# Kernel optimization log

Measured on AMD Instinct MI355X. Metric: run time of the kernel, lower is better.

Reference implementation:

```python
import jax, jax.numpy as jnp
import numpy as np

T, N = 32, 256
HID, NL = 64, 1
D_CH, Hg, Wg = 2, 8, 8            # obs shape (2, 8, 8); d must be 2 to match Conv2d(2*HID, 2*HID)
NSUB, SUBDIM = 6, 3               # subtasks shape (n_subtasks, subtask_dim)
OBS_V, SUB_V, NACT = 16, 20, 6    # vocab sizes; action_space.n = NSUB
OBS_LEN = D_CH * Hg * Wg          # 128
SUB_LEN = NSUB * SUBDIM           # 18
GRU_IN = HID * (OBS_LEN + SUBDIM) # 8384
STATE = 2 + NL * HID + NACT + NSUB  # a(1)+v(1)+h(64)+a_probs(6)+p(6) = 78


def setup_inputs() -> dict:
    key = jax.random.key(0)
    ks = jax.random.split(key, 12)
    obs_idx = jax.random.randint(ks[0], (T, N, OBS_LEN), 0, OBS_V)
    sub_idx = jax.random.randint(ks[1], (T, N, SUB_LEN), 0, SUB_V)
    act = jax.random.randint(ks[2], (T, N, 1), 0, NACT)  # all >= 0 -> sample_new is a no-op
    inputs = jnp.concatenate([obs_idx, sub_idx, act], -1).astype(jnp.float32)
    hx = jnp.zeros((1, N, STATE), jnp.float32)  # all-zero -> new_episode everywhere
    sd = lambda f: 1.0 / np.sqrt(f)
    return dict(
        inputs=inputs,
        hx=hx,
        subtask_emb=jax.random.normal(ks[3], (SUB_V, HID)),
        obs_emb=jax.random.normal(ks[4], (OBS_V, HID)),
        conv_w=jax.random.normal(ks[5], (2 * HID, 2 * HID)) * sd(2 * HID),
        conv_b=jnp.zeros((2 * HID,)),
        w_ih=jax.random.normal(ks[6], (3 * HID, GRU_IN)) * sd(GRU_IN),
        w_hh=jax.random.normal(ks[7], (3 * HID, HID)) * sd(HID),
        b_ih=jnp.zeros((3 * HID,)),
        b_hh=jnp.zeros((3 * HID,)),
        critic_w=jax.random.normal(ks[8], (1, HID)) * sd(HID),
        critic_b=jnp.zeros((1,)),
        phi_w=jax.random.normal(ks[9], (1, HID)) * sd(HID),
        phi_b=jnp.zeros((1,)),
    )


def _forward(inputs, hx, subtask_emb, obs_emb, conv_w, conv_b, w_ih, w_hh,
             b_ih, b_hh, critic_w, critic_b, phi_w, phi_b):
    ints = inputs.astype(jnp.int32)
    obs_all = ints[:, :, :OBS_LEN]                      # (T,N,128)
    sub_all = ints[:, :, OBS_LEN:OBS_LEN + SUB_LEN]     # (T,N,18)
    act_all = ints[:, :, -1]                            # (T,N)

    # subtask memory from first timestep: (N, NSUB, SUBDIM*HID)
    M = subtask_emb[sub_all[0]].reshape(N, NSUB, SUBDIM * HID)

    hx0 = hx[0]
    new_episode = jnp.all(hx0 == 0, axis=-1)            # (N,)
    # recurrent state split order a(1), v(1), h(NL*HID), a_probs(NACT), p(NSUB)
    h0 = hx0[:, 2:2 + NL * HID].reshape(N, NL, HID).transpose(1, 0, 2)  # (NL,N,HID)
    p0 = hx0[:, 2 + NL * HID + NACT:]
    p0 = p0.at[:, 0].set(jnp.where(new_episode, 1.0, p0[:, 0]))

    def gru_cell(x, h):
        gx = x @ w_ih.T + b_ih
        gh = h @ w_hh.T + b_hh
        r = jax.nn.sigmoid(gx[:, :HID] + gh[:, :HID])
        z = jax.nn.sigmoid(gx[:, HID:2 * HID] + gh[:, HID:2 * HID])
        n = jnp.tanh(gx[:, 2 * HID:] + r * gh[:, 2 * HID:])
        return (1 - z) * n + z * h

    def step(carry, xt):
        h, p = carry
        obs_t, act_t = xt
        r_vec = jnp.einsum('ns,nsk->nk', p, M)          # (p.unsqueeze(1) @ M).squeeze(1)
        emb = obs_emb[obs_t.reshape(N, D_CH, Hg, Wg)]   # (N,2,H,W,HID)
        conv_in = emb.transpose(0, 1, 4, 2, 3).reshape(N, 2 * HID, Hg * Wg)
        conv_out = jnp.einsum('ncp,oc->nop', conv_in, conv_w) + conv_b[None, :, None]  # 1x1 conv
        gru_in = jnp.concatenate([conv_out.reshape(N, -1), r_vec], -1)
        hn = gru_cell(gru_in, h[0])                     # single-layer GRU, seq len 1
        h_new = hn[None]
        c = jax.nn.sigmoid(hn @ phi_w.T + phi_b)        # (N,1)
        # torch.roll(F.pad(p,(0,1)), 1) flattened: pad column is 0, so this is a
        # right-shift with 0 fill; p1[:, -1] == p[:, -1].
        p1 = jnp.concatenate([jnp.zeros((N, 1), p.dtype), p[:, :-1]], axis=1)
        p2 = p1 + p * p[:, -1:]
        p_new = (1 - c) * p + c * p2
        probs = p_new / p_new.sum(-1, keepdims=True)    # FixedCategorical(p).probs
        v = hn @ critic_w.T + critic_b                  # (N,1)
        a = act_t.astype(jnp.float32)[:, None]          # actions all >=0 -> no resampling
        h_flat = h_new.transpose(1, 0, 2).reshape(N, -1)
        ys = jnp.concatenate([a, v, h_flat, probs, p_new], -1)
        return (h_new, p_new), ys

    _, hx_out = jax.lax.scan(step, (h0, p0), (obs_all, act_all))  # (T,N,78)
    return hx_out


def reference(inputs, hx, subtask_emb, obs_emb, conv_w, conv_b, w_ih, w_hh,
              b_ih, b_hh, critic_w, critic_b, phi_w, phi_b):
    hx_out = _forward(inputs, hx, subtask_emb, obs_emb, conv_w, conv_b, w_ih,
                      w_hh, b_ih, b_hh, critic_w, critic_b, phi_w, phi_b)
    return (hx_out, hx_out[-1:])
```

## Files before the change

kernel.cpp:

```cpp
#include <hip/hip_runtime.h>
#include <hip/hip_bf16.h>
#include <math.h>

#define TT 32
#define NN 256
#define HID 64
#define OBS_LEN 128
#define SUB_LEN 18
#define IN_ROW 147
#define GJ 192
#define GRU_IN 8384
#define STATE 78
#define NSUB 6
#define NT_TILES 1572

typedef __fp16 half2_t __attribute__((ext_vector_type(2)));

__device__ __forceinline__ float sigm(float x) {
    return 1.0f / (1.0f + __expf(-x));
}

__device__ __forceinline__ unsigned short f2bf(float f) {
    unsigned u = __float_as_uint(f);
    u += 0x7fffu + ((u >> 16) & 1u);
    return (unsigned short)(u >> 16);
}

#if defined(__has_builtin)
#if __has_builtin(__builtin_amdgcn_fdot2)
#define HAVE_FDOT2 1
#endif
#endif

__device__ __forceinline__ float fdot2(half2_t a, half2_t b, float c) {
#ifdef HAVE_FDOT2
    return __builtin_amdgcn_fdot2(a, b, c, false);
#else
    return fmaf((float)a.x, (float)b.x, fmaf((float)a.y, (float)b.y, c));
#endif
}

__global__ __launch_bounds__(256) void k_TGC(const float* __restrict__ w_ih,
                                             const float* __restrict__ obs_emb,
                                             const float* __restrict__ conv_w,
                                             const float* __restrict__ conv_b,
                                             const float* __restrict__ b_ih,
                                             float* __restrict__ wT,
                                             float* __restrict__ G,
                                             float* __restrict__ CB2) {
    int b = blockIdx.x;
    int tid = threadIdx.x;
    __shared__ float tile[32][33];
    __shared__ float red[4];

    if (b < NT_TILES) {
        int bx = b % 262, by = b / 262;
        int i0 = bx * 32, j0 = by * 32;
        int tx = tid & 31, ty = tid >> 5;
        #pragma unroll
        for (int a = 0; a < 4; a++)
            tile[ty + a * 8][tx] = w_ih[(size_t)(j0 + ty + a * 8) * GRU_IN + i0 + tx];
        __syncthreads();
        #pragma unroll
        for (int a = 0; a < 4; a++)
            wT[(size_t)(i0 + ty + a * 8) * GJ + j0 + tx] = tile[tx][ty + a * 8];
    } else if (b < NT_TILES + 16) {
        int i = (b - NT_TILES) * 256 + tid;
        int v = i & 15, d = (i >> 4) & 1, o = i >> 5;
        float acc = 0.f;
        const float* oe = obs_emb + v * 64;
        const float* cw = conv_w + o * 128 + d * 64;
        #pragma unroll
        for (int hd = 0; hd < 64; hd++) acc = fmaf(oe[hd], cw[hd], acc);
        G[i] = acc;
    } else {
        int j = b - (NT_TILES + 16);
        const float* wr = w_ih + (size_t)j * GRU_IN;
        float acc = 0.f;
        #pragma unroll 8
        for (int i = tid; i < 8192; i += 256) acc = fmaf(conv_b[i >> 6], wr[i], acc);
        for (int off = 32; off > 0; off >>= 1) acc += __shfl_down(acc, off, 64);
        if ((tid & 63) == 0) red[tid >> 6] = acc;
        __syncthreads();
        if (tid == 0) CB2[j] = b_ih[j] + red[0] + red[1] + red[2] + red[3];
    }
}

__global__ __launch_bounds__(192) void k_EQ(const float* __restrict__ inputs,
                                            const float* __restrict__ subtask_emb,
                                            const float* __restrict__ G,
                                            const float* __restrict__ wT,
                                            unsigned short* __restrict__ E16,
                                            float* __restrict__ Q) {
    int b = blockIdx.x;
    int j = threadIdx.x;

    if (b < 256) {
        int dp = b >> 1, half = b & 1;
        int d = dp >> 6, p = dp & 63;
        __shared__ __align__(16) float Gs[128 * 8];
        for (int e = j; e < 1024; e += GJ) {
            int o = e >> 3, vv = e & 7;
            Gs[e] = G[(o << 5) + (d << 4) + (half << 3) + vv];
        }
        __syncthreads();
        float acc[8];
        #pragma unroll
        for (int v = 0; v < 8; v++) acc[v] = 0.f;
        const float* wb = wT + (size_t)p * GJ + j;
        #pragma unroll 8
        for (int o = 0; o < 128; o++) {
            float w = wb[(size_t)(o * 64) * GJ];
            float4 g0 = *(const float4*)&Gs[o * 8];
            float4 g1 = *(const float4*)&Gs[o * 8 + 4];
            acc[0] = fmaf(g0.x, w, acc[0]);
            acc[1] = fmaf(g0.y, w, acc[1]);
            acc[2] = fmaf(g0.z, w, acc[2]);
            acc[3] = fmaf(g0.w, w, acc[3]);
            acc[4] = fmaf(g1.x, w, acc[4]);
            acc[5] = fmaf(g1.y, w, acc[5]);
            acc[6] = fmaf(g1.z, w, acc[6]);
            acc[7] = fmaf(g1.w, w, acc[7]);
        }
        unsigned short* Eo = E16 + ((size_t)(dp * 16 + half * 8)) * GJ;
        #pragma unroll
        for (int v = 0; v < 8; v++) Eo[v * GJ + j] = f2bf(acc[v]);
    } else {
        int n = b - 256;
        __shared__ int sidx[SUB_LEN];
        __shared__ __align__(16) float Ms[GJ * 8];
        if (j < SUB_LEN) sidx[j] = (int)inputs[(size_t)n * IN_ROW + OBS_LEN + j];
        __syncthreads();
        for (int e = j; e < NSUB * GJ; e += GJ) {
            int s = e / GJ, k = e - s * GJ;
            int row = sidx[s * 3 + (k >> 6)];
            Ms[k * 8 + s] = subtask_emb[row * 64 + (k & 63)];
        }
        __syncthreads();
        float acc[NSUB] = {0.f, 0.f, 0.f, 0.f, 0.f, 0.f};
        const float* base = wT + (size_t)8192 * GJ + j;
        #pragma unroll 8
        for (int k = 0; k < GJ; k++) {
            float w = base[(size_t)k * GJ];
            float4 m0 = *(const float4*)&Ms[k * 8];
            float2 m1 = *(const float2*)&Ms[k * 8 + 4];
            acc[0] = fmaf(m0.x, w, acc[0]);
            acc[1] = fmaf(m0.y, w, acc[1]);
            acc[2] = fmaf(m0.z, w, acc[2]);
            acc[3] = fmaf(m0.w, w, acc[3]);
            acc[4] = fmaf(m1.x, w, acc[4]);
            acc[5] = fmaf(m1.y, w, acc[5]);
        }
        for (int s = 0; s < NSUB; s++) Q[((size_t)n * NSUB + s) * GJ + j] = acc[s];
    }
}

__global__ __launch_bounds__(192) void k_gx(const float* __restrict__ inputs,
                                            const unsigned short* __restrict__ E16,
                                            const float* __restrict__ CB2,
                                            float* __restrict__ gx_all) {
    int tn0 = blockIdx.x * 4;
    int tid = threadIdx.x;
    __shared__ int idx[4][OBS_LEN];
    for (int e = tid; e < 4 * OBS_LEN; e += 192)
        idx[e >> 7][e & 127] = (int)inputs[(size_t)(tn0 + (e >> 7)) * IN_ROW + (e & 127)];
    __syncthreads();
    int r = tid / 48, l = tid - r * 48;
    int jj = l * 4;
    int tn = tn0 + r;
    float4 cb = *(const float4*)(CB2 + jj);
    float a0 = cb.x, a1 = cb.y, a2 = cb.z, a3 = cb.w;
    const int* id = idx[r];
    #pragma unroll 16
    for (int dp = 0; dp < OBS_LEN; dp++) {
        uint2 u = *(const uint2*)(E16 + ((size_t)(dp * 16 + id[dp])) * GJ + jj);
        a0 += __uint_as_float(u.x << 16);
        a1 += __uint_as_float(u.x & 0xffff0000u);
        a2 += __uint_as_float(u.y << 16);
        a3 += __uint_as_float(u.y & 0xffff0000u);
    }
    float4 o4; o4.x = a0; o4.y = a1; o4.z = a2; o4.w = a3;
    *(float4*)(gx_all + (size_t)tn * GJ + jj) = o4;
}

__global__ __launch_bounds__(64, 1) void k_rec(const float* __restrict__ inputs,
                                               const float* __restrict__ hx,
                                               const float* __restrict__ w_hh,
                                               const float* __restrict__ b_hh,
                                               const float* __restrict__ critic_w,
                                               const float* __restrict__ critic_b,
                                               const float* __restrict__ phi_w,
                                               const float* __restrict__ phi_b,
                                               const float* __restrict__ Q,
                                               const float* __restrict__ gx_all,
                                               float* __restrict__ out) {
    int n = blockIdx.x;
    int lane = threadIdx.x;

    __shared__ __align__(16) float gx_lds[TT * GJ];
    __shared__ __align__(16) __fp16 h16[64];
    __shared__ float act_sh[TT];

    for (int e = lane * 4; e < TT * GJ; e += 64 * 4) {
        int t = e / GJ, j = e - t * GJ;
        *(float4*)&gx_lds[e] = *(const float4*)(gx_all + ((size_t)t * NN + n) * GJ + j);
    }
    if (lane < TT)
        act_sh[lane] = inputs[((size_t)lane * NN + n) * IN_ROW + (IN_ROW - 1)];

    half2_t wv0[32], wv1[32], wv2[32];
    {
        const float4* r0 = (const float4*)(w_hh + (size_t)lane * 64);
        const float4* r1 = (const float4*)(w_hh + (size_t)(64 + lane) * 64);
        const float4* r2 = (const float4*)(w_hh + (size_t)(128 + lane) * 64);
        #pragma unroll
        for (int h4 = 0; h4 < 16; h4++) {
            float4 a = r0[h4];
            wv0[2*h4]   = __builtin_amdgcn_cvt_pkrtz(a.x, a.y);
            wv0[2*h4+1] = __builtin_amdgcn_cvt_pkrtz(a.z, a.w);
            float4 c = r1[h4];
            wv1[2*h4]   = __builtin_amdgcn_cvt_pkrtz(c.x, c.y);
            wv1[2*h4+1] = __builtin_amdgcn_cvt_pkrtz(c.z, c.w);
            float4 d = r2[h4];
            wv2[2*h4]   = __builtin_amdgcn_cvt_pkrtz(d.x, d.y);
            wv2[2*h4+1] = __builtin_amdgcn_cvt_pkrtz(d.z, d.w);
        }
    }
    half2_t ph[32];
    {
        const float4* pp = (const float4*)phi_w;
        #pragma unroll
        for (int h4 = 0; h4 < 16; h4++) {
            float4 a = pp[h4];
            ph[2*h4]   = __builtin_amdgcn_cvt_pkrtz(a.x, a.y);
            ph[2*h4+1] = __builtin_amdgcn_cvt_pkrtz(a.z, a.w);
        }
    }
    float q0[NSUB], q1[NSUB], q2[NSUB];
    #pragma unroll
    for (int s = 0; s < NSUB; s++) {
        const float* qb = Q + ((size_t)n * NSUB + s) * GJ;
        q0[s] = qb[lane]; q1[s] = qb[64 + lane]; q2[s] = qb[128 + lane];
    }
    float bh0 = b_hh[lane], bh1 = b_hh[64 + lane], bh2 = b_hh[128 + lane];
    float cw_own = critic_w[lane];
    float phib = phi_b[0], crtb = critic_b[0];

    float v0 = hx[(size_t)n * STATE + lane];
    float v1 = (lane < STATE - 64) ? hx[(size_t)n * STATE + 64 + lane] : 0.f;
    unsigned long long bal0 = __ballot(v0 != 0.f);
    unsigned long long bal1 = __ballot((lane < STATE - 64) && v1 != 0.f);
    bool ne = ((bal0 | bal1) == 0ULL);
    float h_own = hx[(size_t)n * STATE + 2 + lane];
    float p0, p1, p2, p3, p4, p5;
    {
        const float* pb = hx + (size_t)n * STATE + 72;
        p0 = pb[0]; p1 = pb[1]; p2 = pb[2]; p3 = pb[3]; p4 = pb[4]; p5 = pb[5];
    }
    if (ne) p0 = 1.0f;
    h16[lane] = (__fp16)h_own;

    float vlast = 0.f;

    auto finalize = [&](int tf, float pc) {
        float c = sigm(pc + phib);
        float n0 = fmaf(c, (p0 * p5)      - p0, p0);
        float n1 = fmaf(c, (p0 + p1 * p5) - p1, p1);
        float n2 = fmaf(c, (p1 + p2 * p5) - p2, p2);
        float n3 = fmaf(c, (p2 + p3 * p5) - p3, p3);
        float n4 = fmaf(c, (p3 + p4 * p5) - p4, p4);
        float n5 = fmaf(c, (p4 + p5 * p5) - p5, p5);
        float psum = ((n0 + n1) + (n2 + n3)) + (n4 + n5);
        float rinv = 1.0f / psum;
        if (lane < 12) {
            int s = (lane < 6) ? lane : lane - 6;
            float pp = n0;
            pp = (s == 1) ? n1 : pp;
            pp = (s == 2) ? n2 : pp;
            pp = (s == 3) ? n3 : pp;
            pp = (s == 4) ? n4 : pp;
            pp = (s == 5) ? n5 : pp;
            size_t fb = ((size_t)tf * NN + n) * STATE;
            out[fb + ((lane < 6) ? (72 + lane) : (66 + lane - 6))] =
                (lane < 6) ? pp : pp * rinv;
        }
        p0 = n0; p1 = n1; p2 = n2; p3 = n3; p4 = n4; p5 = n5;
    };

    for (int t = 0; t < TT; t++) {
        uint4 raw[8];
        #pragma unroll
        for (int rix = 0; rix < 8; rix++) raw[rix] = ((const uint4*)h16)[rix];
        half2_t h2[32];
        {
            const unsigned* rw = (const unsigned*)raw;
            #pragma unroll
            for (int k = 0; k < 32; k++) h2[k] = __builtin_bit_cast(half2_t, rw[k]);
        }

        float A0 = 0.f, B0 = 0.f, A1 = 0.f, B1 = 0.f, A2 = 0.f, B2 = 0.f;
        float PA = 0.f, PB = 0.f;
        #pragma unroll
        for (int k = 0; k < 16; k++) {
            A0 = fdot2(h2[k], wv0[k], A0);
            B0 = fdot2(h2[16 + k], wv0[16 + k], B0);
            A1 = fdot2(h2[k], wv1[k], A1);
            B1 = fdot2(h2[16 + k], wv1[16 + k], B1);
            A2 = fdot2(h2[k], wv2[k], A2);
            B2 = fdot2(h2[16 + k], wv2[16 + k], B2);
            PA = fdot2(h2[k], ph[k], PA);
            PB = fdot2(h2[16 + k], ph[16 + k], PB);
        }
        float pc = PA + PB;

        if (t > 0) finalize(t - 1, pc);

        float gx0 = gx_lds[t * GJ + lane];
        float gx1 = gx_lds[t * GJ + 64 + lane];
        float gx2 = gx_lds[t * GJ + 128 + lane];
        gx0 = fmaf(p0, q0[0], gx0); gx1 = fmaf(p0, q1[0], gx1); gx2 = fmaf(p0, q2[0], gx2);
        gx0 = fmaf(p1, q0[1], gx0); gx1 = fmaf(p1, q1[1], gx1); gx2 = fmaf(p1, q2[1], gx2);
        gx0 = fmaf(p2, q0[2], gx0); gx1 = fmaf(p2, q1[2], gx1); gx2 = fmaf(p2, q2[2], gx2);
        gx0 = fmaf(p3, q0[3], gx0); gx1 = fmaf(p3, q1[3], gx1); gx2 = fmaf(p3, q2[3], gx2);
        gx0 = fmaf(p4, q0[4], gx0); gx1 = fmaf(p4, q1[4], gx1); gx2 = fmaf(p4, q2[4], gx2);
        gx0 = fmaf(p5, q0[5], gx0); gx1 = fmaf(p5, q1[5], gx1); gx2 = fmaf(p5, q2[5], gx2);

        float gh0 = bh0 + A0 + B0;
        float gh1 = bh1 + A1 + B1;
        float gh2 = bh2 + A2 + B2;

        float r = sigm(gx0 + gh0);
        float z = sigm(gx1 + gh1);
        float x2 = fmaf(r, gh2, gx2);
        float e2 = __expf(2.f * x2);
        float nv = 1.f - 2.f / (e2 + 1.f);
        float hn = fmaf(z, h_own - nv, nv);

        size_t base = ((size_t)t * NN + n) * STATE;
        out[base + 2 + lane] = hn;
        float vc = hn * cw_own;
        #pragma unroll
        for (int off = 32; off > 0; off >>= 1) vc += __shfl_xor(vc, off, 64);
        vlast = vc + crtb;
        if (lane == 0) out[base + 1] = vlast;
        else if (lane == 1) out[base + 0] = act_sh[t];

        h16[lane] = (__fp16)hn;
        h_own = hn;
    }

    {
        uint4 raw[8];
        #pragma unroll
        for (int rix = 0; rix < 8; rix++) raw[rix] = ((const uint4*)h16)[rix];
        const unsigned* rw = (const unsigned*)raw;
        float PA = 0.f, PB = 0.f;
        #pragma unroll
        for (int k = 0; k < 16; k++) {
            PA = fdot2(__builtin_bit_cast(half2_t, rw[k]), ph[k], PA);
            PB = fdot2(__builtin_bit_cast(half2_t, rw[16 + k]), ph[16 + k], PB);
        }
        finalize(TT - 1, PA + PB);
        float psum = ((p0 + p1) + (p2 + p3)) + (p4 + p5);
        float rinv = 1.0f / psum;
        size_t fs = (size_t)TT * NN * STATE + (size_t)n * STATE;
        out[fs + 2 + lane] = h_own;
        if (lane < 12) {
            int s = (lane < 6) ? lane : lane - 6;
            float pp = p0;
            pp = (s == 1) ? p1 : pp;
            pp = (s == 2) ? p2 : pp;
            pp = (s == 3) ? p3 : pp;
            pp = (s == 4) ? p4 : pp;
            pp = (s == 5) ? p5 : pp;
            out[fs + ((lane < 6) ? (72 + lane) : (66 + lane - 6))] =
                (lane < 6) ? pp : pp * rinv;
        } else if (lane == 12) {
            out[fs + 0] = act_sh[TT - 1];
        } else if (lane == 13) {
            out[fs + 1] = vlast;
        }
    }
}

extern "C" void kernel_launch(void* const* d_in, const int* in_sizes, int n_in,
                              void* d_out, int out_size, void* d_ws, size_t ws_size,
                              hipStream_t stream) {
    const float* inputs      = (const float*)d_in[0];
    const float* hx          = (const float*)d_in[1];
    const float* subtask_emb = (const float*)d_in[2];
    const float* obs_emb     = (const float*)d_in[3];
    const float* conv_w      = (const float*)d_in[4];
    const float* conv_b      = (const float*)d_in[5];
    const float* w_ih        = (const float*)d_in[6];
    const float* w_hh        = (const float*)d_in[7];
    const float* b_ih        = (const float*)d_in[8];
    const float* b_hh        = (const float*)d_in[9];
    const float* critic_w    = (const float*)d_in[10];
    const float* critic_b    = (const float*)d_in[11];
    const float* phi_w       = (const float*)d_in[12];
    const float* phi_b       = (const float*)d_in[13];
    float* out = (float*)d_out;

    float* ws   = (float*)d_ws;
    float* wT   = ws;
    float* G    = wT + (size_t)GRU_IN * GJ;
    float* CB2  = G + 4096;
    float* Ef   = CB2 + 192;
    unsigned short* E16 = (unsigned short*)Ef;
    float* Q    = Ef + 196608;
    float* gx   = Q + (size_t)NN * NSUB * GJ;

    k_TGC<<<NT_TILES + 16 + GJ, 256, 0, stream>>>(w_ih, obs_emb, conv_w, conv_b,
                                                  b_ih, wT, G, CB2);
    k_EQ<<<512, GJ, 0, stream>>>(inputs, subtask_emb, G, wT, E16, Q);
    k_gx<<<TT * NN / 4, GJ, 0, stream>>>(inputs, E16, CB2, gx);
    k_rec<<<NN, 64, 0, stream>>>(inputs, hx, w_hh, b_hh, critic_w, critic_b,
                                 phi_w, phi_b, Q, gx, out);
}
```

Measured before the change: 178.3 us.

## Precompute gather byte offsets in k_gx and defer critic reduction out of recurrence

```diff
diff --git a/kernel.cpp b/kernel.cpp
--- a/kernel.cpp
+++ b/kernel.cpp
@@ -161,25 +161,66 @@
                                             float* __restrict__ gx_all) {
     int tn0 = blockIdx.x * 4;
     int tid = threadIdx.x;
-    __shared__ int idx[4][OBS_LEN];
-    for (int e = tid; e < 4 * OBS_LEN; e += 192)
-        idx[e >> 7][e & 127] = (int)inputs[(size_t)(tn0 + (e >> 7)) * IN_ROW + (e & 127)];
+    __shared__ __align__(16) int off[4][OBS_LEN];
+    for (int e = tid; e < 4 * OBS_LEN; e += 192) {
+        int row = e >> 7, dp = e & 127;
+        int id = (int)inputs[(size_t)(tn0 + row) * IN_ROW + dp];
+        off[row][dp] = (dp * 16 + id) * 384;
+    }
     __syncthreads();
     int r = tid / 48, l = tid - r * 48;
     int jj = l * 4;
     int tn = tn0 + r;
-    float4 cb = *(const float4*)(CB2 + jj);
-    float a0 = cb.x, a1 = cb.y, a2 = cb.z, a3 = cb.w;
-    const int* id = idx[r];
-    #pragma unroll 16
-    for (int dp = 0; dp < OBS_LEN; dp++) {
-        uint2 u = *(const uint2*)(E16 + ((size_t)(dp * 16 + id[dp])) * GJ + jj);
-        a0 += __uint_as_float(u.x << 16);
-        a1 += __uint_as_float(u.x & 0xffff0000u);
-        a2 += __uint_as_float(u.y << 16);
-        a3 += __uint_as_float(u.y & 0xffff0000u);
-    }
-    float4 o4; o4.x = a0; o4.y = a1; o4.z = a2; o4.w = a3;
+    const char* base = (const char*)E16 + jj * 2;
+    float2 acc0 = *(const float2*)(CB2 + jj);
+    float2 acc1 = *(const float2*)(CB2 + jj + 2);
+    const int* id = off[r];
+    #pragma unroll
+    for (int dq = 0; dq < 16; dq++) {
+        int4 o0 = *(const int4*)&id[dq * 8];
+        int4 o1 = *(const int4*)&id[dq * 8 + 4];
+        uint2 u0 = *(const uint2*)(base + o0.x);
+        uint2 u1 = *(const uint2*)(base + o0.y);
+        uint2 u2 = *(const uint2*)(base + o0.z);
+        uint2 u3 = *(const uint2*)(base + o0.w);
+        uint2 u4 = *(const uint2*)(base + o1.x);
+        uint2 u5 = *(const uint2*)(base + o1.y);
+        uint2 u6 = *(const uint2*)(base + o1.z);
+        uint2 u7 = *(const uint2*)(base + o1.w);
+        acc0.x += __uint_as_float(u0.x << 16);
+        acc0.y += __uint_as_float(u0.x & 0xffff0000u);
+        acc1.x += __uint_as_float(u0.y << 16);
+        acc1.y += __uint_as_float(u0.y & 0xffff0000u);
+        acc0.x += __uint_as_float(u1.x << 16);
+        acc0.y += __uint_as_float(u1.x & 0xffff0000u);
+        acc1.x += __uint_as_float(u1.y << 16);
+        acc1.y += __uint_as_float(u1.y & 0xffff0000u);
+        acc0.x += __uint_as_float(u2.x << 16);
+        acc0.y += __uint_as_float(u2.x & 0xffff0000u);
+        acc1.x += __uint_as_float(u2.y << 16);
+        acc1.y += __uint_as_float(u2.y & 0xffff0000u);
+        acc0.x += __uint_as_float(u3.x << 16);
+        acc0.y += __uint_as_float(u3.x & 0xffff0000u);
+        acc1.x += __uint_as_float(u3.y << 16);
+        acc1.y += __uint_as_float(u3.y & 0xffff0000u);
+        acc0.x += __uint_as_float(u4.x << 16);
+        acc0.y += __uint_as_float(u4.x & 0xffff0000u);
+        acc1.x += __uint_as_float(u4.y << 16);
+        acc1.y += __uint_as_float(u4.y & 0xffff0000u);
+        acc0.x += __uint_as_float(u5.x << 16);
+        acc0.y += __uint_as_float(u5.x & 0xffff0000u);
+        acc1.x += __uint_as_float(u5.y << 16);
+        acc1.y += __uint_as_float(u5.y & 0xffff0000u);
+        acc0.x += __uint_as_float(u6.x << 16);
+        acc0.y += __uint_as_float(u6.x & 0xffff0000u);
+        acc1.x += __uint_as_float(u6.y << 16);
+        acc1.y += __uint_as_float(u6.y & 0xffff0000u);
+        acc0.x += __uint_as_float(u7.x << 16);
+        acc0.y += __uint_as_float(u7.x & 0xffff0000u);
+        acc1.x += __uint_as_float(u7.y << 16);
+        acc1.y += __uint_as_float(u7.y & 0xffff0000u);
+    }
+    float4 o4; o4.x = acc0.x; o4.y = acc0.y; o4.z = acc1.x; o4.w = acc1.y;
     *(float4*)(gx_all + (size_t)tn * GJ + jj) = o4;
 }
 
@@ -199,6 +240,8 @@
 
     __shared__ __align__(16) float gx_lds[TT * GJ];
     __shared__ __align__(16) __fp16 h16[64];
+    __shared__ float h_all[TT][65];
+    __shared__ float cw_sh[64];
     __shared__ float act_sh[TT];
 
     for (int e = lane * 4; e < TT * GJ; e += 64 * 4) {
@@ -243,7 +286,7 @@
         q0[s] = qb[lane]; q1[s] = qb[64 + lane]; q2[s] = qb[128 + lane];
     }
     float bh0 = b_hh[lane], bh1 = b_hh[64 + lane], bh2 = b_hh[128 + lane];
-    float cw_own = critic_w[lane];
+    cw_sh[lane] = critic_w[lane];
     float phib = phi_b[0], crtb = critic_b[0];
 
     float v0 = hx[(size_t)n * STATE + lane];
@@ -259,8 +302,6 @@
     }
     if (ne) p0 = 1.0f;
     h16[lane] = (__fp16)h_own;
-
-    float vlast = 0.f;
 
     auto finalize = [&](int tf, float pc) {
         float c = sigm(pc + phib);
@@ -338,14 +379,10 @@
 
         size_t base = ((size_t)t * NN + n) * STATE;
         out[base + 2 + lane] = hn;
-        float vc = hn * cw_own;
-        #pragma unroll
-        for (int off = 32; off > 0; off >>= 1) vc += __shfl_xor(vc, off, 64);
-        vlast = vc + crtb;
-        if (lane == 0) out[base + 1] = vlast;
-        else if (lane == 1) out[base + 0] = act_sh[t];
+        if (lane == 1) out[base + 0] = act_sh[t];
 
         h16[lane] = (__fp16)hn;
+        h_all[t][lane] = hn;
         h_own = hn;
     }
 
@@ -361,6 +398,23 @@
             PB = fdot2(__builtin_bit_cast(half2_t, rw[16 + k]), ph[16 + k], PB);
         }
         finalize(TT - 1, PA + PB);
+    }
+
+    float vlast;
+    {
+        int tp = lane >> 1, half = lane & 1;
+        const float* hr = &h_all[tp][half * 32];
+        const float* cr = &cw_sh[half * 32];
+        float vc = 0.f;
+        #pragma unroll
+        for (int k = 0; k < 32; k++) vc = fmaf(hr[k], cr[k], vc);
+        vc += __shfl_xor(vc, 1, 64);
+        float vt = vc + crtb;
+        if (half == 0) out[((size_t)tp * NN + n) * STATE + 1] = vt;
+        vlast = __shfl(vt, 62, 64);
+    }
+
+    {
         float psum = ((p0 + p1) + (p2 + p3)) + (p4 + p5);
         float rinv = 1.0f / psum;
         size_t fs = (size_t)TT * NN * STATE + (size_t)n * STATE;
```

Result: faster. 160.2 us (-10.2%).
